# Kernel tuning notes

Hardware: AMD Instinct MI355X
Metric: run time of the kernel (lower is better)

The kernel has to match this reference:

```python
import jax, jax.numpy as jnp
import numpy as np

N, D, K, H = 100000, 128, 16, 8
EPS = 1e-5


def setup_inputs() -> dict:
    key = jax.random.key(0)
    ks = jax.random.split(key, 8)
    s = 0.02
    return {
        "x": jax.random.normal(ks[0], (N, D), jnp.float32),
        "attention_samples": jax.random.randint(ks[1], (N, K), 0, N),
        "in_proj_w": jax.random.normal(ks[2], (3 * D, D), jnp.float32) * s,
        "in_proj_b": jnp.zeros((3 * D,), jnp.float32),
        "out_w": jax.random.normal(ks[3], (D, D), jnp.float32) * s,
        "out_b": jnp.zeros((D,), jnp.float32),
        "w1": jax.random.normal(ks[4], (4 * D, D), jnp.float32) * s,
        "b1": jnp.zeros((4 * D,), jnp.float32),
        "w2": jax.random.normal(ks[5], (D, 4 * D), jnp.float32) * s,
        "b2": jnp.zeros((D,), jnp.float32),
        "g1": jnp.ones((D,), jnp.float32),
        "be1": jnp.zeros((D,), jnp.float32),
        "g2": jnp.ones((D,), jnp.float32),
        "be2": jnp.zeros((D,), jnp.float32),
    }


def _layernorm(x, g, b):
    m = jnp.mean(x, axis=-1, keepdims=True)
    v = jnp.mean(jnp.square(x - m), axis=-1, keepdims=True)
    return (x - m) * jax.lax.rsqrt(v + EPS) * g + b


def reference(x, attention_samples, in_proj_w, in_proj_b, out_w, out_b,
              w1, b1, w2, b2, g1, be1, g2, be2):
    n, d = x.shape
    h = H
    hd = d // h
    wq, wk, wv = jnp.split(in_proj_w, 3, axis=0)
    bq, bk, bv = jnp.split(in_proj_b, 3, axis=0)
    # per-node query (q_len = 1)
    q = (x @ wq.T + bq).reshape(n, h, hd)            # [N,H,hd]
    samp = x[attention_samples]                       # [N,K,D] gathered neighbors
    k_ = (samp @ wk.T + bk).reshape(n, -1, h, hd)     # [N,K,H,hd]
    v_ = (samp @ wv.T + bv).reshape(n, -1, h, hd)
    scores = jnp.einsum('nhd,nkhd->nhk', q, k_) / jnp.sqrt(jnp.float32(hd))
    attn = jax.nn.softmax(scores, axis=-1)
    ctx = jnp.einsum('nhk,nkhd->nhd', attn, v_).reshape(n, d)
    attn_out = ctx @ out_w.T + out_b
    y = _layernorm(x + attn_out, g1, be1)
    ff = jax.nn.relu(y @ w1.T + b1) @ w2.T + b2
    return _layernorm(y + ff, g2, be2)
```

## Files before the change

### kernel.cpp

```cpp
#include <hip/hip_runtime.h>
#include <hip/hip_bf16.h>

typedef __attribute__((ext_vector_type(8))) short short8;
typedef __attribute__((ext_vector_type(4))) float f32x4;
typedef __attribute__((ext_vector_type(2))) float f32x2;

#define EPS 1e-5f

__device__ __forceinline__ unsigned short f2bf(float f) {
    union { float f; unsigned u; } v; v.f = f;
    unsigned u = v.u;
    u += 0x7FFFu + ((u >> 16) & 1u);
    return (unsigned short)(u >> 16);
}
__device__ __forceinline__ float bflo(unsigned u) {
    union { unsigned u; float f; } v; v.u = u << 16; return v.f;
}
__device__ __forceinline__ float bfhi(unsigned u) {
    union { unsigned u; float f; } v; v.u = u & 0xffff0000u; return v.f;
}
__device__ __forceinline__ float bf2f(ushort u) {
    union { unsigned u; float f; } v; v.u = ((unsigned)u) << 16; return v.f;
}
__device__ __forceinline__ unsigned char f2fp8(float v) {
    return (unsigned char)(__builtin_amdgcn_cvt_pk_fp8_f32(v, v, 0, false) & 0xff);
}
__device__ __forceinline__ unsigned pk4fp8(float a, float b, float c, float d) {
    unsigned u = __builtin_amdgcn_cvt_pk_fp8_f32(a, b, 0, false);
    u = __builtin_amdgcn_cvt_pk_fp8_f32(c, d, u, true);
    return u;
}
__device__ __forceinline__ int sig(int p) {
    return (((p >> 2) & 1) << 4) | (((p >> 3) & 3) << 2) | (p & 3);
}

__device__ __forceinline__ short8 load_frag_f32(const float* __restrict__ p) {
    f32x4 a = *(const f32x4*)p;
    f32x4 b = *(const f32x4*)(p + 4);
    short8 r;
    r[0] = (short)f2bf(a[0]); r[1] = (short)f2bf(a[1]);
    r[2] = (short)f2bf(a[2]); r[3] = (short)f2bf(a[3]);
    r[4] = (short)f2bf(b[0]); r[5] = (short)f2bf(b[1]);
    r[6] = (short)f2bf(b[2]); r[7] = (short)f2bf(b[3]);
    return r;
}

__device__ __forceinline__ float dot16_q_k8(const ushort* q, const unsigned char* kp) {
    uint4 kw = *(const uint4*)kp;
    const unsigned* qd = (const unsigned*)q;
    f32x2 a, b; float s = 0.f;
    a = __builtin_amdgcn_cvt_pk_f32_fp8(kw.x, false);
    b = __builtin_amdgcn_cvt_pk_f32_fp8(kw.x, true);
    s += a[0]*bflo(qd[0]) + a[1]*bfhi(qd[0]) + b[0]*bflo(qd[1]) + b[1]*bfhi(qd[1]);
    a = __builtin_amdgcn_cvt_pk_f32_fp8(kw.y, false);
    b = __builtin_amdgcn_cvt_pk_f32_fp8(kw.y, true);
    s += a[0]*bflo(qd[2]) + a[1]*bfhi(qd[2]) + b[0]*bflo(qd[3]) + b[1]*bfhi(qd[3]);
    a = __builtin_amdgcn_cvt_pk_f32_fp8(kw.z, false);
    b = __builtin_amdgcn_cvt_pk_f32_fp8(kw.z, true);
    s += a[0]*bflo(qd[4]) + a[1]*bfhi(qd[4]) + b[0]*bflo(qd[5]) + b[1]*bfhi(qd[5]);
    a = __builtin_amdgcn_cvt_pk_f32_fp8(kw.w, false);
    b = __builtin_amdgcn_cvt_pk_f32_fp8(kw.w, true);
    s += a[0]*bflo(qd[6]) + a[1]*bfhi(qd[6]) + b[0]*bflo(qd[7]) + b[1]*bfhi(qd[7]);
    return s;
}

__global__ __launch_bounds__(256) void k_prep(
        const float* __restrict__ ipw, const float* __restrict__ ow,
        const float* __restrict__ w1, const float* __restrict__ w2,
        ushort* __restrict__ wqb, unsigned char* __restrict__ wcat8) {
    int i = blockIdx.x * 256 + threadIdx.x;
    if (i < 49152) wqb[i] = f2bf(ipw[i]);
    if (i < 147456) {
        float v;
        if (i < 16384) {
            int r = i >> 7, s = (i >> 3) & 15, e = i & 7;
            v = ow[r*128 + ((s ^ (r & 15)) << 3) + e];
        } else if (i < 81920) {
            int j = i - 16384;
            int kb = j >> 12, r = (j >> 7) & 31, s = (j >> 3) & 15, e = j & 7;
            int cp = ((s ^ (r & 15)) << 3) + e;
            int cs = (cp & ~31) | sig(cp & 31);
            v = w1[(kb*32 + r)*128 + cs];
        } else {
            int j = i - 81920;
            int kb = j >> 12, ch = (j >> 10) & 3, rw = (j >> 3) & 127, e = j & 7;
            v = w2[rw*512 + kb*32 + sig(ch*8 + e)];
        }
        wcat8[i] = f2fp8(16.f * v);
    }
}

__global__ __launch_bounds__(256) void k_qkv(
        const float* __restrict__ x, const ushort* __restrict__ w,
        const float* __restrict__ bias, ushort* __restrict__ qt,
        unsigned char* __restrict__ kv8, ushort* __restrict__ xb, int N) {
    __shared__ ushort sls[64 * 392];
    const int wave = threadIdx.x >> 6, lane = threadIdx.x & 63;
    const int l16 = lane & 15, l4 = lane >> 4;
    const int base = blockIdx.x * 64;

    short8 af[4][4];
    #pragma unroll
    for (int mt = 0; mt < 4; ++mt) {
        int row = base + mt*16 + l16;
        int rc = row < N ? row : N - 1;
        const float* p = x + (size_t)rc*128 + l4*8;
        #pragma unroll
        for (int kb = 0; kb < 4; ++kb) af[mt][kb] = load_frag_f32(p + kb*32);
    }
    #pragma unroll
    for (int mt = 0; mt < 4; ++mt) {
        int row = base + mt*16 + l16;
        if (row < N) {
            #pragma unroll
            for (int kb = 0; kb < 4; ++kb)
                *(short8*)(xb + (size_t)row*128 + kb*32 + l4*8) = af[mt][kb];
        }
    }
    #pragma unroll
    for (int i = 0; i < 6; ++i) {
        int col = (wave*6 + i)*16 + l16;
        const ushort* pw = w + (size_t)col*128 + l4*8;
        short8 bf[4];
        #pragma unroll
        for (int kb = 0; kb < 4; ++kb) bf[kb] = *(const short8*)(pw + kb*32);
        float bv = bias[col];
        #pragma unroll
        for (int mt = 0; mt < 4; ++mt) {
            f32x4 acc = {0.f, 0.f, 0.f, 0.f};
            #pragma unroll
            for (int kb = 0; kb < 4; ++kb)
                acc = __builtin_amdgcn_mfma_f32_16x16x32_bf16(af[mt][kb], bf[kb], acc, 0, 0, 0);
            #pragma unroll
            for (int r = 0; r < 4; ++r)
                sls[(mt*16 + l4*4 + r)*392 + col] = f2bf(acc[r] + bv);
        }
    }
    __syncthreads();
    {
        const int row = threadIdx.x >> 2, q = threadIdx.x & 3;
        const int grow = base + row;
        if (grow < N) {
            const ushort* sp = sls + row*392;
            #pragma unroll
            for (int j = 0; j < 4; ++j) {
                uint4 v = *(const uint4*)(sp + q*32 + j*8);
                *(uint4*)(qt + (size_t)grow*128 + q*32 + j*8) = v;
            }
            #pragma unroll
            for (int j = 0; j < 4; ++j) {
                unsigned wds[4];
                #pragma unroll
                for (int h = 0; h < 4; ++h) {
                    const ushort* e = sp + 128 + q*64 + j*16 + h*4;
                    wds[h] = pk4fp8(bf2f(e[0]), bf2f(e[1]), bf2f(e[2]), bf2f(e[3]));
                }
                *(uint4*)(kv8 + (size_t)grow*256 + q*64 + j*16) =
                    make_uint4(wds[0], wds[1], wds[2], wds[3]);
            }
        }
    }
}

__global__ __launch_bounds__(256) void k_attn(
        ushort* __restrict__ qt, const unsigned char* __restrict__ kv8,
        const int* __restrict__ samp, int N) {
    __shared__ float aw[4][8][17];
    __shared__ int   ai[4][16];
    const int wave = threadIdx.x >> 6, lane = threadIdx.x & 63;
    const int n = blockIdx.x * 4 + wave;
    if (n >= N) return;
    const int k  = lane & 15;
    const int hp = lane >> 4;
    const int h0 = hp, h1 = hp + 4;

    const int idx = samp[(size_t)n*16 + k];
    const ushort* qrow = qt + (size_t)n*128;
    const unsigned char* krow = kv8 + (size_t)idx*256;

    float s0 = dot16_q_k8(qrow + h0*16, krow + h0*16);
    float s1 = dot16_q_k8(qrow + h1*16, krow + h1*16);
    s0 *= 0.25f; s1 *= 0.25f;
    float m0 = s0, m1 = s1;
    #pragma unroll
    for (int off = 1; off < 16; off <<= 1) {
        m0 = fmaxf(m0, __shfl_xor(m0, off));
        m1 = fmaxf(m1, __shfl_xor(m1, off));
    }
    float e0 = __expf(s0 - m0), e1 = __expf(s1 - m1);
    float d0 = e0, d1 = e1;
    #pragma unroll
    for (int off = 1; off < 16; off <<= 1) {
        d0 += __shfl_xor(d0, off);
        d1 += __shfl_xor(d1, off);
    }
    aw[wave][h0][k] = e0 / d0;
    aw[wave][h1][k] = e1 / d1;
    if (hp == 0) ai[wave][k] = idx;

    const int c = lane & 15;
    const int g = lane >> 4;
    const int h = c >> 1;

    int rows[4];
    #pragma unroll
    for (int b = 0; b < 4; ++b) rows[b] = ai[wave][g + b*4];
    uint2 vv[4];
    #pragma unroll
    for (int b = 0; b < 4; ++b)
        vv[b] = *(const uint2*)(kv8 + (size_t)(unsigned)rows[b]*256 + 128 + c*8);
    float wk[4];
    #pragma unroll
    for (int b = 0; b < 4; ++b) wk[b] = aw[wave][h][g + b*4];

    float a8[8] = {0.f,0.f,0.f,0.f,0.f,0.f,0.f,0.f};
    #pragma unroll
    for (int b = 0; b < 4; ++b) {
        f32x2 p;
        p = __builtin_amdgcn_cvt_pk_f32_fp8(vv[b].x, false);
        a8[0] = fmaf(wk[b], p[0], a8[0]); a8[1] = fmaf(wk[b], p[1], a8[1]);
        p = __builtin_amdgcn_cvt_pk_f32_fp8(vv[b].x, true);
        a8[2] = fmaf(wk[b], p[0], a8[2]); a8[3] = fmaf(wk[b], p[1], a8[3]);
        p = __builtin_amdgcn_cvt_pk_f32_fp8(vv[b].y, false);
        a8[4] = fmaf(wk[b], p[0], a8[4]); a8[5] = fmaf(wk[b], p[1], a8[5]);
        p = __builtin_amdgcn_cvt_pk_f32_fp8(vv[b].y, true);
        a8[6] = fmaf(wk[b], p[0], a8[6]); a8[7] = fmaf(wk[b], p[1], a8[7]);
    }
    #pragma unroll
    for (int i = 0; i < 8; ++i) {
        a8[i] += __shfl_xor(a8[i], 16);
        a8[i] += __shfl_xor(a8[i], 32);
    }
    if (lane < 16) {
        unsigned lo = pk4fp8(8.f*a8[0], 8.f*a8[1], 8.f*a8[2], 8.f*a8[3]);
        unsigned hi = pk4fp8(8.f*a8[4], 8.f*a8[5], 8.f*a8[6], 8.f*a8[7]);
        *(uint2*)((unsigned char*)qt + (size_t)n*256 + c*8) = make_uint2(lo, hi);
    }
}

__global__ __launch_bounds__(512) void k_tail(
        const unsigned char* __restrict__ ctx8, const float* __restrict__ ob,
        const ushort* __restrict__ xb,
        const float* __restrict__ g1, const float* __restrict__ be1,
        const unsigned char* __restrict__ wcat8, const float* __restrict__ b1,
        const float* __restrict__ b2,
        const float* __restrict__ g2, const float* __restrict__ be2,
        float* __restrict__ out, int N) {
    __shared__ __align__(16) unsigned char smem[147456];
    const int tid = threadIdx.x;
    const int wave = tid >> 6, lane = tid & 63;
    const int l16 = lane & 15, l4 = lane >> 4;

    {
        const uint4* src = (const uint4*)wcat8;
        #pragma unroll
        for (int b = 0; b < 3; ++b) {
            uint4 v[6];
            #pragma unroll
            for (int j = 0; j < 6; ++j) v[j] = src[(b*6 + j)*512 + tid];
            #pragma unroll
            for (int j = 0; j < 6; ++j)
                *(uint4*)(smem + ((size_t)(b*6 + j)*512 + tid)*16) = v[j];
        }
    }
    __syncthreads();

    const int ntiles = (N + 31) >> 5;
    const int nwv = gridDim.x * 8;
    for (int t = blockIdx.x * 8 + wave; t < ntiles; t += nwv) {
        int row[2], rc[2];
        row[0] = t*32 + l16;      rc[0] = row[0] < N ? row[0] : N - 1;
        row[1] = t*32 + 16 + l16; rc[1] = row[1] < N ? row[1] : N - 1;

        long cf[2][4];
        #pragma unroll
        for (int mt = 0; mt < 2; ++mt)
            #pragma unroll
            for (int c = 0; c < 4; ++c)
                cf[mt][c] = *(const long*)(ctx8 + (size_t)rc[mt]*256 + c*32 + l4*8);
        f32x4 acc[2][8];
        #pragma unroll
        for (int mt = 0; mt < 2; ++mt)
            #pragma unroll
            for (int nt = 0; nt < 8; ++nt) acc[mt][nt] = (f32x4){0.f,0.f,0.f,0.f};
        #pragma unroll
        for (int nt = 0; nt < 8; ++nt) {
            #pragma unroll
            for (int c = 0; c < 4; ++c) {
                long wf = *(const long*)(smem + (nt*16 + l16)*128 + (((c*4 + l4) ^ l16) << 3));
                acc[0][nt] = __builtin_amdgcn_mfma_f32_16x16x32_fp8_fp8(wf, cf[0][c], acc[0][nt], 0, 0, 0);
                acc[1][nt] = __builtin_amdgcn_mfma_f32_16x16x32_fp8_fp8(wf, cf[1][c], acc[1][nt], 0, 0, 0);
            }
        }

        float sum0 = 0.f, sq0 = 0.f, sum1 = 0.f, sq1 = 0.f;
        #pragma unroll
        for (int nt = 0; nt < 8; ++nt) {
            f32x4 obv = *(const f32x4*)(ob + nt*16 + l4*4);
            uint2 xr0 = *(const uint2*)(xb + (size_t)rc[0]*128 + nt*16 + l4*4);
            uint2 xr1 = *(const uint2*)(xb + (size_t)rc[1]*128 + nt*16 + l4*4);
            acc[0][nt][0] = acc[0][nt][0]*(1.f/128.f) + obv[0] + bflo(xr0.x);
            acc[0][nt][1] = acc[0][nt][1]*(1.f/128.f) + obv[1] + bfhi(xr0.x);
            acc[0][nt][2] = acc[0][nt][2]*(1.f/128.f) + obv[2] + bflo(xr0.y);
            acc[0][nt][3] = acc[0][nt][3]*(1.f/128.f) + obv[3] + bfhi(xr0.y);
            acc[1][nt][0] = acc[1][nt][0]*(1.f/128.f) + obv[0] + bflo(xr1.x);
            acc[1][nt][1] = acc[1][nt][1]*(1.f/128.f) + obv[1] + bfhi(xr1.x);
            acc[1][nt][2] = acc[1][nt][2]*(1.f/128.f) + obv[2] + bflo(xr1.y);
            acc[1][nt][3] = acc[1][nt][3]*(1.f/128.f) + obv[3] + bfhi(xr1.y);
            #pragma unroll
            for (int r = 0; r < 4; ++r) {
                sum0 += acc[0][nt][r]; sq0 += acc[0][nt][r]*acc[0][nt][r];
                sum1 += acc[1][nt][r]; sq1 += acc[1][nt][r]*acc[1][nt][r];
            }
        }
        sum0 += __shfl_xor(sum0, 16); sum0 += __shfl_xor(sum0, 32);
        sq0  += __shfl_xor(sq0, 16);  sq0  += __shfl_xor(sq0, 32);
        sum1 += __shfl_xor(sum1, 16); sum1 += __shfl_xor(sum1, 32);
        sq1  += __shfl_xor(sq1, 16);  sq1  += __shfl_xor(sq1, 32);
        float mean[2], rstd[2];
        mean[0] = sum0 * (1.f/128.f);
        rstd[0] = rsqrtf(sq0*(1.f/128.f) - mean[0]*mean[0] + EPS);
        mean[1] = sum1 * (1.f/128.f);
        rstd[1] = rsqrtf(sq1*(1.f/128.f) - mean[1]*mean[1] + EPS);

        short8 yf16[2][4];
        long   yf8[2][4];
        #pragma unroll
        for (int mt = 0; mt < 2; ++mt) {
            #pragma unroll
            for (int c = 0; c < 4; ++c) {
                float yv[8];
                #pragma unroll
                for (int half = 0; half < 2; ++half) {
                    int nt = 2*c + half;
                    f32x4 gv = *(const f32x4*)(g1 + nt*16 + l4*4);
                    f32x4 bv = *(const f32x4*)(be1 + nt*16 + l4*4);
                    #pragma unroll
                    for (int r = 0; r < 4; ++r) {
                        float yn = (acc[mt][nt][r] - mean[mt]) * rstd[mt] * gv[r] + bv[r];
                        yv[half*4 + r] = yn;
                        yf16[mt][c][half*4 + r] = (short)f2bf(yn);
                    }
                }
                unsigned lo = pk4fp8(yv[0], yv[1], yv[2], yv[3]);
                unsigned hi = pk4fp8(yv[4], yv[5], yv[6], yv[7]);
                yf8[mt][c] = (long)(((unsigned long long)hi << 32) | lo);
            }
        }

        f32x4 acc2[2][8];
        #pragma unroll
        for (int mt = 0; mt < 2; ++mt)
            #pragma unroll
            for (int nt = 0; nt < 8; ++nt) acc2[mt][nt] = (f32x4){0.f,0.f,0.f,0.f};
        #pragma unroll 4
        for (int kb = 0; kb < 16; ++kb) {
            const unsigned char* w1b = smem + 16384 + kb*4096;
            long wA[4], wB[4];
            #pragma unroll
            for (int c = 0; c < 4; ++c) {
                int so = ((c*4 + l4) ^ l16) << 3;
                wA[c] = *(const long*)(w1b + l16*128 + so);
                wB[c] = *(const long*)(w1b + (16 + l16)*128 + so);
            }
            f32x4 hA[2] = {{0.f,0.f,0.f,0.f},{0.f,0.f,0.f,0.f}};
            f32x4 hB[2] = {{0.f,0.f,0.f,0.f},{0.f,0.f,0.f,0.f}};
            #pragma unroll
            for (int c = 0; c < 4; ++c)
                #pragma unroll
                for (int mt = 0; mt < 2; ++mt) {
                    hA[mt] = __builtin_amdgcn_mfma_f32_16x16x32_fp8_fp8(wA[c], yf8[mt][c], hA[mt], 0, 0, 0);
                    hB[mt] = __builtin_amdgcn_mfma_f32_16x16x32_fp8_fp8(wB[c], yf8[mt][c], hB[mt], 0, 0, 0);
                }
            f32x4 bA = *(const f32x4*)(b1 + kb*32 + l4*4);
            f32x4 bB = *(const f32x4*)(b1 + kb*32 + 16 + l4*4);
            long hf8[2];
            #pragma unroll
            for (int mt = 0; mt < 2; ++mt) {
                float vA[4], vB[4];
                #pragma unroll
                for (int r = 0; r < 4; ++r) {
                    vA[r] = fmaxf(hA[mt][r]*0.0625f + bA[r], 0.f);
                    vB[r] = fmaxf(hB[mt][r]*0.0625f + bB[r], 0.f);
                }
                unsigned lo = pk4fp8(vA[0], vA[1], vA[2], vA[3]);
                unsigned hi = pk4fp8(vB[0], vB[1], vB[2], vB[3]);
                hf8[mt] = (long)(((unsigned long long)hi << 32) | lo);
            }
            const unsigned char* w2b = smem + 81920 + kb*4096 + l4*1024;
            #pragma unroll
            for (int nt = 0; nt < 8; ++nt) {
                long w2f = *(const long*)(w2b + (nt*16 + l16)*8);
                acc2[0][nt] = __builtin_amdgcn_mfma_f32_16x16x32_fp8_fp8(w2f, hf8[0], acc2[0][nt], 0, 0, 0);
                acc2[1][nt] = __builtin_amdgcn_mfma_f32_16x16x32_fp8_fp8(w2f, hf8[1], acc2[1][nt], 0, 0, 0);
            }
        }

        #pragma unroll
        for (int mt = 0; mt < 2; ++mt) {
            float sum2 = 0.f, sq2 = 0.f;
            #pragma unroll
            for (int nt = 0; nt < 8; ++nt) {
                f32x4 b2v = *(const f32x4*)(b2 + nt*16 + l4*4);
                #pragma unroll
                for (int r = 0; r < 4; ++r) {
                    float s = bf2f((ushort)yf16[mt][nt >> 1][(nt & 1)*4 + r])
                              + acc2[mt][nt][r]*0.0625f + b2v[r];
                    acc2[mt][nt][r] = s; sum2 += s; sq2 += s*s;
                }
            }
            sum2 += __shfl_xor(sum2, 16); sum2 += __shfl_xor(sum2, 32);
            sq2  += __shfl_xor(sq2, 16);  sq2  += __shfl_xor(sq2, 32);
            float mean2 = sum2 * (1.f/128.f);
            float rstd2 = rsqrtf(sq2*(1.f/128.f) - mean2*mean2 + EPS);
            if (row[mt] < N) {
                #pragma unroll
                for (int nt = 0; nt < 8; ++nt) {
                    f32x4 gv = *(const f32x4*)(g2 + nt*16 + l4*4);
                    f32x4 bv = *(const f32x4*)(be2 + nt*16 + l4*4);
                    f32x4 o;
                    #pragma unroll
                    for (int r = 0; r < 4; ++r)
                        o[r] = (acc2[mt][nt][r] - mean2) * rstd2 * gv[r] + bv[r];
                    *(f32x4*)(out + (size_t)row[mt]*128 + nt*16 + l4*4) = o;
                }
            }
        }
    }
}

extern "C" void kernel_launch(void* const* d_in, const int* in_sizes, int n_in,
                              void* d_out, int out_size, void* d_ws, size_t ws_size,
                              hipStream_t stream) {
    (void)n_in; (void)out_size; (void)ws_size;
    const float* x   = (const float*)d_in[0];
    const int*   smp = (const int*)  d_in[1];
    const float* ipw = (const float*)d_in[2];
    const float* ipb = (const float*)d_in[3];
    const float* ow  = (const float*)d_in[4];
    const float* ob  = (const float*)d_in[5];
    const float* w1  = (const float*)d_in[6];
    const float* b1  = (const float*)d_in[7];
    const float* w2  = (const float*)d_in[8];
    const float* b2  = (const float*)d_in[9];
    const float* g1  = (const float*)d_in[10];
    const float* be1 = (const float*)d_in[11];
    const float* g2  = (const float*)d_in[12];
    const float* be2 = (const float*)d_in[13];
    const int N = in_sizes[0] / 128;

    ushort* qt   = (ushort*)d_ws;
    unsigned char* kv8 = (unsigned char*)(qt + (size_t)N*128);
    ushort* wqb  = (ushort*)(kv8 + (size_t)N*256);
    unsigned char* wcat8 = (unsigned char*)(wqb + 49152);
    ushort* xb   = (ushort*)(wcat8 + 147456);
    float*  outp = (float*)d_out;

    k_prep <<<576,       256, 0, stream>>>(ipw, ow, w1, w2, wqb, wcat8);
    k_qkv  <<<(N+63)/64, 256, 0, stream>>>(x, wqb, ipb, qt, kv8, xb, N);
    k_attn <<<(N+3)/4,   256, 0, stream>>>(qt, kv8, smp, N);
    k_tail <<<256,       512, 0, stream>>>((const unsigned char*)qt, ob, xb, g1, be1,
                                           wcat8, b1, b2, g2, be2, outp, N);
}
```

Before: 212.9 us.

## Process 16-row tiles per wave instead of 32 to cut register pressure

```diff
diff --git a/kernel.cpp b/kernel.cpp
--- a/kernel.cpp
+++ b/kernel.cpp
@@ -265,94 +265,72 @@
     }
     __syncthreads();
 
-    const int ntiles = (N + 31) >> 5;
+    const int ntiles = (N + 15) >> 4;
     const int nwv = gridDim.x * 8;
     for (int t = blockIdx.x * 8 + wave; t < ntiles; t += nwv) {
-        int row[2], rc[2];
-        row[0] = t*32 + l16;      rc[0] = row[0] < N ? row[0] : N - 1;
-        row[1] = t*32 + 16 + l16; rc[1] = row[1] < N ? row[1] : N - 1;
-
-        long cf[2][4];
-        #pragma unroll
-        for (int mt = 0; mt < 2; ++mt)
+        const int row = t*16 + l16;
+        const int rc = row < N ? row : N - 1;
+
+        f32x4 acc[8];
+        #pragma unroll
+        for (int nt = 0; nt < 8; ++nt) acc[nt] = (f32x4){0.f,0.f,0.f,0.f};
+        {
+            long cf[4];
             #pragma unroll
             for (int c = 0; c < 4; ++c)
-                cf[mt][c] = *(const long*)(ctx8 + (size_t)rc[mt]*256 + c*32 + l4*8);
-        f32x4 acc[2][8];
-        #pragma unroll
-        for (int mt = 0; mt < 2; ++mt)
-            #pragma unroll
-            for (int nt = 0; nt < 8; ++nt) acc[mt][nt] = (f32x4){0.f,0.f,0.f,0.f};
-        #pragma unroll
-        for (int nt = 0; nt < 8; ++nt) {
-            #pragma unroll
-            for (int c = 0; c < 4; ++c) {
-                long wf = *(const long*)(smem + (nt*16 + l16)*128 + (((c*4 + l4) ^ l16) << 3));
-                acc[0][nt] = __builtin_amdgcn_mfma_f32_16x16x32_fp8_fp8(wf, cf[0][c], acc[0][nt], 0, 0, 0);
-                acc[1][nt] = __builtin_amdgcn_mfma_f32_16x16x32_fp8_fp8(wf, cf[1][c], acc[1][nt], 0, 0, 0);
-            }
-        }
-
-        float sum0 = 0.f, sq0 = 0.f, sum1 = 0.f, sq1 = 0.f;
+                cf[c] = *(const long*)(ctx8 + (size_t)rc*256 + c*32 + l4*8);
+            #pragma unroll
+            for (int nt = 0; nt < 8; ++nt) {
+                #pragma unroll
+                for (int c = 0; c < 4; ++c) {
+                    long wf = *(const long*)(smem + (nt*16 + l16)*128 + (((c*4 + l4) ^ l16) << 3));
+                    acc[nt] = __builtin_amdgcn_mfma_f32_16x16x32_fp8_fp8(wf, cf[c], acc[nt], 0, 0, 0);
+                }
+            }
+        }
+
+        float sum0 = 0.f, sq0 = 0.f;
         #pragma unroll
         for (int nt = 0; nt < 8; ++nt) {
             f32x4 obv = *(const f32x4*)(ob + nt*16 + l4*4);
-            uint2 xr0 = *(const uint2*)(xb + (size_t)rc[0]*128 + nt*16 + l4*4);
-            uint2 xr1 = *(const uint2*)(xb + (size_t)rc[1]*128 + nt*16 + l4*4);
-            acc[0][nt][0] = acc[0][nt][0]*(1.f/128.f) + obv[0] + bflo(xr0.x);
-            acc[0][nt][1] = acc[0][nt][1]*(1.f/128.f) + obv[1] + bfhi(xr0.x);
-            acc[0][nt][2] = acc[0][nt][2]*(1.f/128.f) + obv[2] + bflo(xr0.y);
-            acc[0][nt][3] = acc[0][nt][3]*(1.f/128.f) + obv[3] + bfhi(xr0.y);
-            acc[1][nt][0] = acc[1][nt][0]*(1.f/128.f) + obv[0] + bflo(xr1.x);
-            acc[1][nt][1] = acc[1][nt][1]*(1.f/128.f) + obv[1] + bfhi(xr1.x);
-            acc[1][nt][2] = acc[1][nt][2]*(1.f/128.f) + obv[2] + bflo(xr1.y);
-            acc[1][nt][3] = acc[1][nt][3]*(1.f/128.f) + obv[3] + bfhi(xr1.y);
-            #pragma unroll
-            for (int r = 0; r < 4; ++r) {
-                sum0 += acc[0][nt][r]; sq0 += acc[0][nt][r]*acc[0][nt][r];
-                sum1 += acc[1][nt][r]; sq1 += acc[1][nt][r]*acc[1][nt][r];
-            }
+            uint2 xr = *(const uint2*)(xb + (size_t)rc*128 + nt*16 + l4*4);
+            acc[nt][0] = acc[nt][0]*(1.f/128.f) + obv[0] + bflo(xr.x);
+            acc[nt][1] = acc[nt][1]*(1.f/128.f) + obv[1] + bfhi(xr.x);
+            acc[nt][2] = acc[nt][2]*(1.f/128.f) + obv[2] + bflo(xr.y);
+            acc[nt][3] = acc[nt][3]*(1.f/128.f) + obv[3] + bfhi(xr.y);
+            #pragma unroll
+            for (int r = 0; r < 4; ++r) { sum0 += acc[nt][r]; sq0 += acc[nt][r]*acc[nt][r]; }
         }
         sum0 += __shfl_xor(sum0, 16); sum0 += __shfl_xor(sum0, 32);
         sq0  += __shfl_xor(sq0, 16);  sq0  += __shfl_xor(sq0, 32);
-        sum1 += __shfl_xor(sum1, 16); sum1 += __shfl_xor(sum1, 32);
-        sq1  += __shfl_xor(sq1, 16);  sq1  += __shfl_xor(sq1, 32);
-        float mean[2], rstd[2];
-        mean[0] = sum0 * (1.f/128.f);
-        rstd[0] = rsqrtf(sq0*(1.f/128.f) - mean[0]*mean[0] + EPS);
-        mean[1] = sum1 * (1.f/128.f);
-        rstd[1] = rsqrtf(sq1*(1.f/128.f) - mean[1]*mean[1] + EPS);
-
-        short8 yf16[2][4];
-        long   yf8[2][4];
-        #pragma unroll
-        for (int mt = 0; mt < 2; ++mt) {
-            #pragma unroll
-            for (int c = 0; c < 4; ++c) {
-                float yv[8];
+        float mean = sum0 * (1.f/128.f);
+        float rstd = rsqrtf(sq0*(1.f/128.f) - mean*mean + EPS);
+
+        short8 yf16[4];
+        long   yf8[4];
+        #pragma unroll
+        for (int c = 0; c < 4; ++c) {
+            float yv[8];
+            #pragma unroll
+            for (int half = 0; half < 2; ++half) {
+                int nt = 2*c + half;
+                f32x4 gv = *(const f32x4*)(g1 + nt*16 + l4*4);
+                f32x4 bv = *(const f32x4*)(be1 + nt*16 + l4*4);
                 #pragma unroll
-                for (int half = 0; half < 2; ++half) {
-                    int nt = 2*c + half;
-                    f32x4 gv = *(const f32x4*)(g1 + nt*16 + l4*4);
-                    f32x4 bv = *(const f32x4*)(be1 + nt*16 + l4*4);
-                    #pragma unroll
-                    for (int r = 0; r < 4; ++r) {
-                        float yn = (acc[mt][nt][r] - mean[mt]) * rstd[mt] * gv[r] + bv[r];
-                        yv[half*4 + r] = yn;
-                        yf16[mt][c][half*4 + r] = (short)f2bf(yn);
-                    }
+                for (int r = 0; r < 4; ++r) {
+                    float yn = (acc[nt][r] - mean) * rstd * gv[r] + bv[r];
+                    yv[half*4 + r] = yn;
+                    yf16[c][half*4 + r] = (short)f2bf(yn);
                 }
-                unsigned lo = pk4fp8(yv[0], yv[1], yv[2], yv[3]);
-                unsigned hi = pk4fp8(yv[4], yv[5], yv[6], yv[7]);
-                yf8[mt][c] = (long)(((unsigned long long)hi << 32) | lo);
-            }
-        }
-
-        f32x4 acc2[2][8];
-        #pragma unroll
-        for (int mt = 0; mt < 2; ++mt)
-            #pragma unroll
-            for (int nt = 0; nt < 8; ++nt) acc2[mt][nt] = (f32x4){0.f,0.f,0.f,0.f};
+            }
+            unsigned lo = pk4fp8(yv[0], yv[1], yv[2], yv[3]);
+            unsigned hi = pk4fp8(yv[4], yv[5], yv[6], yv[7]);
+            yf8[c] = (long)(((unsigned long long)hi << 32) | lo);
+        }
+
+        f32x4 (&acc2)[8] = acc;
+        #pragma unroll
+        for (int nt = 0; nt < 8; ++nt) acc2[nt] = (f32x4){0.f,0.f,0.f,0.f};
         #pragma unroll 4
         for (int kb = 0; kb < 16; ++kb) {
             const unsigned char* w1b = smem + 16384 + kb*4096;
@@ -363,67 +341,56 @@
                 wA[c] = *(const long*)(w1b + l16*128 + so);
                 wB[c] = *(const long*)(w1b + (16 + l16)*128 + so);
             }
-            f32x4 hA[2] = {{0.f,0.f,0.f,0.f},{0.f,0.f,0.f,0.f}};
-            f32x4 hB[2] = {{0.f,0.f,0.f,0.f},{0.f,0.f,0.f,0.f}};
-            #pragma unroll
-            for (int c = 0; c < 4; ++c)
-                #pragma unroll
-                for (int mt = 0; mt < 2; ++mt) {
-                    hA[mt] = __builtin_amdgcn_mfma_f32_16x16x32_fp8_fp8(wA[c], yf8[mt][c], hA[mt], 0, 0, 0);
-                    hB[mt] = __builtin_amdgcn_mfma_f32_16x16x32_fp8_fp8(wB[c], yf8[mt][c], hB[mt], 0, 0, 0);
-                }
+            f32x4 hA = {0.f,0.f,0.f,0.f}, hB = {0.f,0.f,0.f,0.f};
+            #pragma unroll
+            for (int c = 0; c < 4; ++c) {
+                hA = __builtin_amdgcn_mfma_f32_16x16x32_fp8_fp8(wA[c], yf8[c], hA, 0, 0, 0);
+                hB = __builtin_amdgcn_mfma_f32_16x16x32_fp8_fp8(wB[c], yf8[c], hB, 0, 0, 0);
+            }
             f32x4 bA = *(const f32x4*)(b1 + kb*32 + l4*4);
             f32x4 bB = *(const f32x4*)(b1 + kb*32 + 16 + l4*4);
-            long hf8[2];
-            #pragma unroll
-            for (int mt = 0; mt < 2; ++mt) {
-                float vA[4], vB[4];
-                #pragma unroll
-                for (int r = 0; r < 4; ++r) {
-                    vA[r] = fmaxf(hA[mt][r]*0.0625f + bA[r], 0.f);
-                    vB[r] = fmaxf(hB[mt][r]*0.0625f + bB[r], 0.f);
-                }
-                unsigned lo = pk4fp8(vA[0], vA[1], vA[2], vA[3]);
-                unsigned hi = pk4fp8(vB[0], vB[1], vB[2], vB[3]);
-                hf8[mt] = (long)(((unsigned long long)hi << 32) | lo);
-            }
+            float vA[4], vB[4];
+            #pragma unroll
+            for (int r = 0; r < 4; ++r) {
+                vA[r] = fmaxf(hA[r]*0.0625f + bA[r], 0.f);
+                vB[r] = fmaxf(hB[r]*0.0625f + bB[r], 0.f);
+            }
+            unsigned lo = pk4fp8(vA[0], vA[1], vA[2], vA[3]);
+            unsigned hi = pk4fp8(vB[0], vB[1], vB[2], vB[3]);
+            long hf8 = (long)(((unsigned long long)hi << 32) | lo);
             const unsigned char* w2b = smem + 81920 + kb*4096 + l4*1024;
             #pragma unroll
             for (int nt = 0; nt < 8; ++nt) {
                 long w2f = *(const long*)(w2b + (nt*16 + l16)*8);
-                acc2[0][nt] = __builtin_amdgcn_mfma_f32_16x16x32_fp8_fp8(w2f, hf8[0], acc2[0][nt], 0, 0, 0);
-                acc2[1][nt] = __builtin_amdgcn_mfma_f32_16x16x32_fp8_fp8(w2f, hf8[1], acc2[1][nt], 0, 0, 0);
-            }
-        }
-
-        #pragma unroll
-        for (int mt = 0; mt < 2; ++mt) {
-            float sum2 = 0.f, sq2 = 0.f;
+                acc2[nt] = __builtin_amdgcn_mfma_f32_16x16x32_fp8_fp8(w2f, hf8, acc2[nt], 0, 0, 0);
+            }
+        }
+
+        float sum2 = 0.f, sq2 = 0.f;
+        #pragma unroll
+        for (int nt = 0; nt < 8; ++nt) {
+            f32x4 b2v = *(const f32x4*)(b2 + nt*16 + l4*4);
+            #pragma unroll
+            for (int r = 0; r < 4; ++r) {
+                float s = bf2f((ushort)yf16[nt >> 1][(nt & 1)*4 + r])
+                          + acc2[nt][r]*0.0625f + b2v[r];
+                acc2[nt][r] = s; sum2 += s; sq2 += s*s;
+            }
+        }
+        sum2 += __shfl_xor(sum2, 16); sum2 += __shfl_xor(sum2, 32);
+        sq2  += __shfl_xor(sq2, 16);  sq2  += __shfl_xor(sq2, 32);
+        float mean2 = sum2 * (1.f/128.f);
+        float rstd2 = rsqrtf(sq2*(1.f/128.f) - mean2*mean2 + EPS);
+        if (row < N) {
             #pragma unroll
             for (int nt = 0; nt < 8; ++nt) {
-                f32x4 b2v = *(const f32x4*)(b2 + nt*16 + l4*4);
+                f32x4 gv = *(const f32x4*)(g2 + nt*16 + l4*4);
+                f32x4 bv = *(const f32x4*)(be2 + nt*16 + l4*4);
+                f32x4 o;
                 #pragma unroll
-                for (int r = 0; r < 4; ++r) {
-                    float s = bf2f((ushort)yf16[mt][nt >> 1][(nt & 1)*4 + r])
-                              + acc2[mt][nt][r]*0.0625f + b2v[r];
-                    acc2[mt][nt][r] = s; sum2 += s; sq2 += s*s;
-                }
-            }
-            sum2 += __shfl_xor(sum2, 16); sum2 += __shfl_xor(sum2, 32);
-            sq2  += __shfl_xor(sq2, 16);  sq2  += __shfl_xor(sq2, 32);
-            float mean2 = sum2 * (1.f/128.f);
-            float rstd2 = rsqrtf(sq2*(1.f/128.f) - mean2*mean2 + EPS);
-            if (row[mt] < N) {
-                #pragma unroll
-                for (int nt = 0; nt < 8; ++nt) {
-                    f32x4 gv = *(const f32x4*)(g2 + nt*16 + l4*4);
-                    f32x4 bv = *(const f32x4*)(be2 + nt*16 + l4*4);
-                    f32x4 o;
-                    #pragma unroll
-                    for (int r = 0; r < 4; ++r)
-                        o[r] = (acc2[mt][nt][r] - mean2) * rstd2 * gv[r] + bv[r];
-                    *(f32x4*)(out + (size_t)row[mt]*128 + nt*16 + l4*4) = o;
-                }
+                for (int r = 0; r < 4; ++r)
+                    o[r] = (acc2[nt][r] - mean2) * rstd2 * gv[r] + bv[r];
+                *(f32x4*)(out + (size_t)row*128 + nt*16 + l4*4) = o;
             }
         }
     }
```

Result: slower. 220.9 us (+3.7%).
